# Performance work log

Hardware: AMD Instinct MI355X
Metric: run time of the kernel (lower is better)

## Reference

```python
import jax, jax.numpy as jnp
import numpy as np

B, T, C, E, K = 8, 2048, 1024, 8, 2
CAP = int(T / E * 1.25)  # expert capacity per batch row = 320


def setup_inputs() -> dict:
    key = jax.random.key(0)
    ks = jax.random.split(key, 6)
    s = lambda k, shape, fan: jax.random.normal(k, shape, jnp.float32) / np.sqrt(fan)
    return dict(
        x=jax.random.normal(ks[0], (B, T, C), jnp.float32),
        rw1=s(ks[1], (C, 4 * C), C), rb1=jnp.zeros((4 * C,), jnp.float32),
        rw2=s(ks[2], (4 * C, 4 * C), 4 * C), rb2=jnp.zeros((4 * C,), jnp.float32),
        rw3=s(ks[3], (4 * C, E), 4 * C), rb3=jnp.zeros((E,), jnp.float32),
        ew1=s(ks[4], (E, C, 4 * C), C), eb1=jnp.zeros((E, 4 * C), jnp.float32),
        ew2=s(ks[5], (E, 4 * C, C), 4 * C), eb2=jnp.zeros((E, C), jnp.float32),
    )


def reference(x, rw1, rb1, rw2, rb2, rw3, rb3, ew1, eb1, ew2, eb2):
    # Router (dropout is identity in eval): MLP -> softmax over experts
    h = jax.nn.relu(x @ rw1 + rb1)
    h = jax.nn.relu(h @ rw2 + rb2)
    probs = jax.nn.softmax(h @ rw3 + rb3, axis=-1)        # [B,T,E]
    topk_p, topk_e = jax.lax.top_k(probs, K)              # [B,T,K]

    b_ids = jnp.broadcast_to(jnp.arange(B)[:, None], (B, T))
    out = jnp.zeros_like(x)
    # Loop over small fixed number of experts (mirrors per-rank expert compute)
    for e in range(E):
        sel = (topk_e == e)                               # [B,T,K]
        mask = sel.any(-1)                                # token routed to expert e
        gate = (topk_p * sel).sum(-1)                     # unnormalized top-k prob
        pos = jnp.cumsum(mask, axis=1) - 1                # slot within capacity buffer
        keep = mask & (pos < CAP)                         # capacity truncation (drop overflow)
        pos_s = jnp.where(keep, pos, CAP)                 # CAP is out-of-range -> dropped
        # Dispatch: scatter kept tokens into [B, CAP, C] capacity-padded buffer
        buf = jnp.zeros((B, CAP, C), x.dtype).at[b_ids, pos_s].set(x, mode='drop')
        # Expert FFN on padded buffer
        y = jax.nn.relu(buf @ ew1[e] + eb1[e]) @ ew2[e] + eb2[e]
        # Combine: gather back to token positions, weight by gate
        g = y[b_ids, jnp.where(keep, pos, 0)]
        out = out + gate[..., None] * jnp.where(keep[..., None], g, jnp.zeros((), x.dtype))
    return out
```

## Files before the change

### kernel.cpp

```cpp
#include <hip/hip_runtime.h>
#include <stdint.h>

typedef _Float16 f16;
typedef _Float16 half8 __attribute__((ext_vector_type(8)));
typedef float f32x4 __attribute__((ext_vector_type(4)));

#define NF_MAX 2048
#define THETA  0.02f

__device__ __forceinline__ void gload16(const void* g, void* l) {
  __builtin_amdgcn_global_load_lds(
      (const __attribute__((address_space(1))) void*)g,
      (__attribute__((address_space(3))) void*)l, 16, 0, 0);
}

#define BAR() do { __builtin_amdgcn_s_barrier(); __builtin_amdgcn_sched_barrier(0); } while (0)
#define WAIT_VM8() do { asm volatile("s_waitcnt vmcnt(8)" ::: "memory"); __builtin_amdgcn_sched_barrier(0); } while (0)
#define WAIT_VM0() do { asm volatile("s_waitcnt vmcnt(0)" ::: "memory"); __builtin_amdgcn_sched_barrier(0); } while (0)

template<int EPI, bool SPLIT3>
__launch_bounds__(512, 2)
__global__ void gemm256(const f16* __restrict__ A0, const f16* __restrict__ A1,
                        const f16* __restrict__ B0, const f16* __restrict__ B1,
                        int N, int Kd, int lda, int ldb,
                        const int* __restrict__ rowsrcA, const f16* __restrict__ zeroPage,
                        const float* __restrict__ bias, int bias_stride, int rows_per_exp,
                        f16* __restrict__ oH, int ldo, float* __restrict__ oAcc,
                        const float* __restrict__ w3, float* __restrict__ oLog,
                        const int* __restrict__ nfp)
{
  __shared__ f16 lds[4 * 8192 * 2 + 512];
  f16* sA = lds;
  f16* sB = lds + 4 * 8192;
  f16* sDummy = lds + 8 * 8192;

  const int tid  = threadIdx.x;
  const int lane = tid & 63, w = tid >> 6;
  const int wm = w >> 2, wn = w & 3;

  const int gx  = gridDim.x, gy = gridDim.y;
  const int bid = blockIdx.y * gx + blockIdx.x;
  int by, bx;
  const int scols = gx >> 3;
  const int nst   = scols * (gy >> 2);
  if ((gx & 7) == 0 && (gy & 3) == 0 && (nst & 7) == 0) {
    const int x = bid & 7, j = bid >> 3;
    const int r = j >> 5, jp = j & 31;
    const int s = r * 8 + x;
    const int srow = s / scols, scol = s - srow * scols;
    by = srow * 4 + (jp >> 3);
    bx = scol * 8 + (jp & 7);
  } else {
    const int nwg = gx * gy;
    const int swz = (bid & 7) * (nwg >> 3) + (bid >> 3);
    by = swz / gx; bx = swz - by * gx;
  }
  const int m0  = by * 256, n0 = bx * 256;
  const int k0  = blockIdx.z * Kd;

  if (nfp) {
    int nf = *nfp; nf = nf < NF_MAX ? nf : NF_MAX;
    const int lim = (nf + 255) & ~255;
    if (m0 >= lim) return;
  }

  int e = 0;
  if (rows_per_exp > 0) e = m0 / rows_per_exp;
  const f16* Bh = B0 + (size_t)e * N * ldb;

  const int nk  = Kd >> 6;
  const int NIT = SPLIT3 ? 3 * nk : nk;

  const int sr  = lane & 15;
  const int sk8 = lane >> 4;

  size_t aoff[2], boff[2];
  bool az[2] = { false, false };
  #pragma unroll
  for (int jj = 0; jj < 2; ++jj) {
    const int arow = m0 + (jj * 8 + w) * 16 + sr;
    if (rowsrcA) {
      const int rs = rowsrcA[arow];
      az[jj] = (rs < 0);
      aoff[jj] = az[jj] ? 0 : (size_t)rs * lda;
    } else {
      aoff[jj] = (size_t)arow * lda;
    }
    boff[jj] = (size_t)(n0 + (jj * 8 + w) * 16 + sr) * ldb;
  }

  auto stageA = [&](const f16* base, int kk, int kc, f16* slotBase, bool valid) {
    #pragma unroll
    for (int jj = 0; jj < 2; ++jj) {
      const int mt = jj * 8 + w;
      f16* dst = valid ? (slotBase + mt * 512) : sDummy;
      const f16* src = az[jj] ? zeroPage
                              : base + aoff[jj] + (k0 + kk + kc * 32 + sk8 * 8);
      gload16(src, dst);
    }
  };
  auto stageB = [&](const f16* base, int kk, int kc, f16* slotBase, bool valid) {
    #pragma unroll
    for (int jj = 0; jj < 2; ++jj) {
      const int mt = jj * 8 + w;
      f16* dst = valid ? (slotBase + mt * 512) : sDummy;
      const f16* src = base + boff[jj] + (k0 + kk + kc * 32 + sk8 * 8);
      gload16(src, dst);
    }
  };

  struct It { const f16* Ab; const f16* Bb; int kk, kin, pass; };
  const f16* Ab0 = SPLIT3 ? A1 : A0;
  auto advance = [&](It& s) {
    if (s.kin + 1 < nk) { s.kin++; }
    else if (SPLIT3 && s.pass < 2) {
      s.kin = 0; s.pass++;
      s.Ab = (s.pass == 0) ? A1 : A0;
      s.Bb = (s.pass == 1) ? B1 : Bh;
    }
    s.kk = s.kin << 6;
  };
  It it1 = { Ab0, Bh, 64, 1, 0 };
  It it2 = { Ab0, Bh, 128, 2, 0 };

  stageA(Ab0, 0, 0, &sA[0], true);
  stageB(Bh,  0, 0, &sB[0], true);
  stageA(Ab0, 0, 1, &sA[8192], true);
  stageB(Bh,  0, 1, &sB[8192], true);
  stageA(it1.Ab, it1.kk, 0, &sA[2 * 8192], true);
  stageB(it1.Bb, it1.kk, 0, &sB[2 * 8192], true);
  WAIT_VM8();
  BAR();

  f32x4 acc[8][4] = {};
  const int aBase = wm * 8;
  const int bBase = wn * 4;

  auto mfma16 = [&](half8* af, half8* bf, int moff) {
    __builtin_amdgcn_s_setprio(1);
    #pragma unroll
    for (int mi = 0; mi < 4; ++mi)
      #pragma unroll
      for (int ni = 0; ni < 4; ++ni)
        acc[moff + mi][ni] = __builtin_amdgcn_mfma_f32_16x16x32_f16(
            af[mi], bf[ni], acc[moff + mi][ni], 0, 0, 0);
    __builtin_amdgcn_s_setprio(0);
  };
  auto rdA = [&](half8* dst, int slot, int mtb) {
    #pragma unroll
    for (int mi = 0; mi < 4; ++mi)
      dst[mi] = *(const half8*)&sA[slot * 8192 + (mtb + mi) * 512 + lane * 8];
  };
  auto rdB = [&](half8* dst, int slot) {
    #pragma unroll
    for (int ni = 0; ni < 4; ++ni)
      dst[ni] = *(const half8*)&sB[slot * 8192 + (bBase + ni) * 512 + lane * 8];
  };

  for (int t = 0; t < NIT; ++t) {
    const int sa0 = (2 * t) & 3, sa1 = sa0 ^ 1;
    const bool v1 = (t + 1 < NIT), v2 = (t + 2 < NIT);

    if (SPLIT3 && t == 2 * nk) {
      #pragma unroll
      for (int mi = 0; mi < 8; ++mi)
        #pragma unroll
        for (int ni = 0; ni < 4; ++ni)
          acc[mi][ni] = acc[mi][ni] * 2.44140625e-4f;
    }

    half8 aF[4], bF[4], aG[4];

    rdA(aF, sa0, aBase);
    rdB(bF, sa0);
    stageA(it1.Ab, it1.kk, 1, &sA[(sa0 ^ 3) * 8192], v1);
    BAR();
    mfma16(aF, bF, 0);
    BAR();

    rdA(aG, sa0, aBase + 4);
    stageB(it1.Bb, it1.kk, 1, &sB[(sa0 ^ 3) * 8192], v1);
    WAIT_VM8();
    BAR();
    mfma16(aG, bF, 4);
    BAR();

    rdA(aF, sa1, aBase);
    rdB(bF, sa1);
    stageA(it2.Ab, it2.kk, 0, &sA[sa0 * 8192], v2);
    BAR();
    mfma16(aF, bF, 0);
    BAR();

    rdA(aG, sa1, aBase + 4);
    stageB(it2.Bb, it2.kk, 0, &sB[sa0 * 8192], v2);
    WAIT_VM8();
    BAR();
    mfma16(aG, bF, 4);
    BAR();

    it1 = it2;
    advance(it2);
  }
  WAIT_VM0();

  float bv[4] = { 0.f, 0.f, 0.f, 0.f };
  if (bias) {
    #pragma unroll
    for (int ni = 0; ni < 4; ++ni) {
      const int col = n0 + wn * 64 + ni * 16 + (lane & 15);
      bv[ni] = bias[(size_t)e * bias_stride + col];
    }
  }

  if (EPI == 2) {
    f32x4 wlo[4], whi[4];
    #pragma unroll
    for (int ni = 0; ni < 4; ++ni) {
      const int col = n0 + wn * 64 + ni * 16 + (lane & 15);
      wlo[ni] = *(const f32x4*)(w3 + (size_t)col * 8);
      whi[ni] = *(const f32x4*)(w3 + (size_t)col * 8 + 4);
    }
    const int p = (n0 >> 8) * 4 + wn;
    #pragma unroll
    for (int mi = 0; mi < 8; ++mi) {
      #pragma unroll
      for (int r = 0; r < 4; ++r) {
        const int row = m0 + wm * 128 + mi * 16 + (lane >> 4) * 4 + r;
        f32x4 plo = {}, phi = {};
        #pragma unroll
        for (int ni = 0; ni < 4; ++ni) {
          const float v = fmaxf(acc[mi][ni][r] + bv[ni], 0.f);
          plo += v * wlo[ni];
          phi += v * whi[ni];
        }
        #pragma unroll
        for (int msk = 1; msk < 16; msk <<= 1) {
          #pragma unroll
          for (int q = 0; q < 4; ++q) {
            plo[q] += __shfl_xor(plo[q], msk);
            phi[q] += __shfl_xor(phi[q], msk);
          }
        }
        if ((lane & 15) == 0) {
          float* dst = oLog + ((size_t)p * ldo + row) * 8;
          *(f32x4*)dst = plo;
          *(f32x4*)(dst + 4) = phi;
        }
      }
    }
  } else {
    #pragma unroll
    for (int mi = 0; mi < 8; ++mi) {
      #pragma unroll
      for (int r = 0; r < 4; ++r) {
        const int row = m0 + wm * 128 + mi * 16 + (lane >> 4) * 4 + r;
        #pragma unroll
        for (int ni = 0; ni < 4; ++ni) {
          const int col = n0 + wn * 64 + ni * 16 + (lane & 15);
          if (EPI == 3) {
            atomicAdd(&oAcc[(size_t)row * ldo + col], acc[mi][ni][r]);
          } else {
            float v = acc[mi][ni][r] + bv[ni];
            if (EPI == 0) v = fmaxf(v, 0.f);
            oH[(size_t)row * ldo + col] = (f16)v;
          }
        }
      }
    }
  }
}

__global__ void split_x(const float* __restrict__ x, f16* __restrict__ hi,
                        f16* __restrict__ lo, int n)
{
  const int i = blockIdx.x * 256 + threadIdx.x;
  if (i * 8 >= n) return;
  const f32x4 a = ((const f32x4*)x)[2 * i];
  const f32x4 b = ((const f32x4*)x)[2 * i + 1];
  half8 h, l;
  #pragma unroll
  for (int j = 0; j < 4; ++j) {
    float v = a[j]; f16 hh = (f16)v;
    h[j] = hh; l[j] = (f16)((v - (float)hh) * 4096.0f);
    v = b[j]; hh = (f16)v;
    h[4 + j] = hh; l[4 + j] = (f16)((v - (float)hh) * 4096.0f);
  }
  ((half8*)hi)[i] = h;
  ((half8*)lo)[i] = l;
}

template<bool SPLIT>
__global__ void transpose_conv(const float* __restrict__ in, f16* __restrict__ oh,
                               f16* __restrict__ ol, int R, int Cc)
{
  __shared__ float tile[64][65];
  const size_t boff = (size_t)blockIdx.z * R * Cc;
  in += boff; oh += boff;
  if (SPLIT) ol += boff;
  const int c0 = blockIdx.x * 64, r0 = blockIdx.y * 64;
  #pragma unroll
  for (int i = 0; i < 16; ++i) {
    const int idx = i * 256 + threadIdx.x;
    const int r = idx >> 6, c = idx & 63;
    tile[r][c] = in[(size_t)(r0 + r) * Cc + (c0 + c)];
  }
  __syncthreads();
  #pragma unroll
  for (int i = 0; i < 16; ++i) {
    const int idx = i * 256 + threadIdx.x;
    const int ro = idx >> 6, co = idx & 63;
    const float v = tile[co][ro];
    const f16 h = (f16)v;
    const size_t o = (size_t)(c0 + ro) * R + (r0 + co);
    oh[o] = h;
    if (SPLIT) ol[o] = (f16)((v - (float)h) * 4096.0f);
  }
}

__global__ void topk_flag(const float* __restrict__ part, const float* __restrict__ b3,
                          int* __restrict__ eidx, float* __restrict__ gval,
                          int* __restrict__ flags, int* __restrict__ nfc)
{
  const int t = blockIdx.x * 256 + threadIdx.x;
  float l[8];
  #pragma unroll
  for (int e = 0; e < 8; ++e) l[e] = b3[e];
  for (int p = 0; p < 64; ++p) {
    const float* src = part + ((size_t)p * 16384 + t) * 8;
    const f32x4 a = *(const f32x4*)src;
    const f32x4 b = *(const f32x4*)(src + 4);
    #pragma unroll
    for (int q = 0; q < 4; ++q) { l[q] += a[q]; l[4 + q] += b[q]; }
  }
  float mx = l[0];
  #pragma unroll
  for (int e = 1; e < 8; ++e) mx = fmaxf(mx, l[e]);
  float ex[8], s = 0.f;
  #pragma unroll
  for (int e = 0; e < 8; ++e) { ex[e] = expf(l[e] - mx); s += ex[e]; }
  float p1 = -1.f, p2 = -1.f; int e1 = 0, e2 = 0;
  #pragma unroll
  for (int e = 0; e < 8; ++e) {
    const float pe = ex[e] / s;
    if (pe > p1)      { p2 = p1; e2 = e1; p1 = pe; e1 = e; }
    else if (pe > p2) { p2 = pe; e2 = e; }
  }
  eidx[t * 2] = e1; eidx[t * 2 + 1] = e2;
  gval[t * 2] = p1; gval[t * 2 + 1] = p2;
  float l1 = -1e30f, l2 = -1e30f, l3 = -1e30f;
  #pragma unroll
  for (int e = 0; e < 8; ++e) {
    const float le = l[e];
    if (le > l1)      { l3 = l2; l2 = l1; l1 = le; }
    else if (le > l2) { l3 = l2; l2 = le; }
    else if (le > l3) { l3 = le; }
  }
  if (l2 - l3 < THETA) {
    const int s0 = atomicAdd(nfc, 1);
    if (s0 < NF_MAX) flags[s0] = t;
  }
}

__global__ void post1(const float* __restrict__ h1r, const float* __restrict__ b1,
                      f16* __restrict__ hh, f16* __restrict__ hl,
                      const int* __restrict__ nfc)
{
  int nf = *nfc; nf = nf < NF_MAX ? nf : NF_MAX;
  const int lim = (nf + 255) & ~255;
  const int row = blockIdx.x;
  if (row >= lim) return;
  const int j = blockIdx.y * 2048 + threadIdx.x * 8;
  const float* src = h1r + (size_t)row * 4096 + j;
  const f32x4 a = *(const f32x4*)src;
  const f32x4 b = *(const f32x4*)(src + 4);
  half8 h, l;
  #pragma unroll
  for (int k = 0; k < 4; ++k) {
    float v = fmaxf(a[k] + b1[j + k], 0.f);
    f16 x = (f16)v; h[k] = x; l[k] = (f16)((v - (float)x) * 4096.0f);
    v = fmaxf(b[k] + b1[j + 4 + k], 0.f);
    x = (f16)v; h[4 + k] = x; l[4 + k] = (f16)((v - (float)x) * 4096.0f);
  }
  *(half8*)(hh + (size_t)row * 4096 + j) = h;
  *(half8*)(hl + (size_t)row * 4096 + j) = l;
}

__global__ void logits_exact(const float* __restrict__ h2r, const float* __restrict__ b2,
                             const float* __restrict__ w3, const float* __restrict__ b3,
                             const int* __restrict__ flags, const int* __restrict__ nfc,
                             int* __restrict__ eidx, float* __restrict__ gval)
{
  const int srow = blockIdx.x;
  int nf = *nfc; nf = nf < NF_MAX ? nf : NF_MAX;
  if (srow >= nf) return;
  const float* hrow = h2r + (size_t)srow * 4096;
  double p[8];
  #pragma unroll
  for (int e = 0; e < 8; ++e) p[e] = 0.0;
  for (int i = 0; i < 16; ++i) {
    const int k = i * 256 + threadIdx.x;
    const double h = (double)fmaxf(hrow[k] + b2[k], 0.f);
    const float* wp = w3 + (size_t)k * 8;
    #pragma unroll
    for (int e = 0; e < 8; ++e) p[e] += h * (double)wp[e];
  }
  #pragma unroll
  for (int e = 0; e < 8; ++e)
    for (int off = 32; off > 0; off >>= 1)
      p[e] += __shfl_down(p[e], off);
  __shared__ double sp[4][8];
  const int lane = threadIdx.x & 63, wv = threadIdx.x >> 6;
  if (lane == 0) {
    #pragma unroll
    for (int e = 0; e < 8; ++e) sp[wv][e] = p[e];
  }
  __syncthreads();
  if (threadIdx.x == 0) {
    float l[8];
    #pragma unroll
    for (int e = 0; e < 8; ++e)
      l[e] = (float)(sp[0][e] + sp[1][e] + sp[2][e] + sp[3][e] + (double)b3[e]);
    float mx = l[0];
    for (int e = 1; e < 8; ++e) mx = fmaxf(mx, l[e]);
    float ex[8], s = 0.f;
    for (int e = 0; e < 8; ++e) { ex[e] = expf(l[e] - mx); s += ex[e]; }
    float p1 = -1.f, p2 = -1.f; int e1 = 0, e2 = 0;
    for (int e = 0; e < 8; ++e) {
      const float pe = ex[e] / s;
      if (pe > p1)      { p2 = p1; e2 = e1; p1 = pe; e1 = e; }
      else if (pe > p2) { p2 = pe; e2 = e; }
    }
    const int tok = flags[srow];
    eidx[tok * 2] = e1; eidx[tok * 2 + 1] = e2;
    gval[tok * 2] = p1; gval[tok * 2 + 1] = p2;
  }
}

__global__ void route_scan(const int* __restrict__ eidx, const float* __restrict__ gval,
                           int* __restrict__ cnt, int* __restrict__ rowsrc,
                           int* __restrict__ tokslot)
{
  const int pair = blockIdx.x;
  const int e = pair >> 3, b = pair & 7;
  const int lane = threadIdx.x;
  int running = 0;
  for (int t0 = 0; t0 < 2048; t0 += 64) {
    const int t = t0 + lane;
    const int i2 = (b * 2048 + t) * 2;
    const int m0 = (eidx[i2] == e), m1 = (eidx[i2 + 1] == e);
    const int m = m0 | m1;
    const unsigned long long bal = __ballot(m);
    const int pos = running + __popcll(bal & ((1ull << lane) - 1ull));
    if (m && pos < 320) {
      const int slot = pair * 320 + pos;
      rowsrc[slot] = b * 2048 + t;
      tokslot[(b * 2048 + t) * 2 + (m0 ? 0 : 1)] = slot;
    }
    running += __popcll(bal);
  }
  const int c = running < 320 ? running : 320;
  for (int s = c + lane; s < 320; s += 64) rowsrc[pair * 320 + s] = -1;
  if (lane == 0) cnt[pair] = c;
}

__global__ void combine(const f16* __restrict__ yb, const int* __restrict__ tokslot,
                        const float* __restrict__ gval, float* __restrict__ out)
{
  const int t = blockIdx.x;
  const int s0 = tokslot[t * 2], s1 = tokslot[t * 2 + 1];
  const float g0 = gval[t * 2], g1 = gval[t * 2 + 1];
  float a[8] = {};
  if (s0 >= 0) {
    const half8 y = ((const half8*)(yb + (size_t)s0 * 1024))[threadIdx.x];
    #pragma unroll
    for (int k = 0; k < 8; ++k) a[k] += g0 * (float)y[k];
  }
  if (s1 >= 0) {
    const half8 y = ((const half8*)(yb + (size_t)s1 * 1024))[threadIdx.x];
    #pragma unroll
    for (int k = 0; k < 8; ++k) a[k] += g1 * (float)y[k];
  }
  float* dst = out + (size_t)t * 1024 + threadIdx.x * 8;
  f32x4 lo = { a[0], a[1], a[2], a[3] }, hi = { a[4], a[5], a[6], a[7] };
  *(f32x4*)dst = lo;
  *(f32x4*)(dst + 4) = hi;
}

extern "C" void kernel_launch(void* const* d_in, const int* in_sizes, int n_in,
                              void* d_out, int out_size, void* d_ws, size_t ws_size,
                              hipStream_t stream)
{
  (void)in_sizes; (void)n_in; (void)out_size;
  const float* x   = (const float*)d_in[0];
  const float* rw1 = (const float*)d_in[1];
  const float* rb1 = (const float*)d_in[2];
  const float* rw2 = (const float*)d_in[3];
  const float* rb2 = (const float*)d_in[4];
  const float* rw3 = (const float*)d_in[5];
  const float* rb3 = (const float*)d_in[6];
  const float* ew1 = (const float*)d_in[7];
  const float* eb1 = (const float*)d_in[8];
  const float* ew2 = (const float*)d_in[9];
  const float* eb2 = (const float*)d_in[10];

  constexpr size_t MB = 1024ull * 1024ull;
  constexpr size_t KB = 1024ull;
  char* ws = (char*)d_ws;
  if (ws_size < 401 * MB) return;

  f16*   h1f  = (f16*)(ws);
  f16*   ew1t = (f16*)(ws);
  f16*   ew2t = (f16*)(ws + 64 * MB);
  f16*   xhi  = (f16*)(ws + 128 * MB);
  char*  S    = ws + 160 * MB;
  int*   eidx   = (int*)(S);
  float* gval   = (float*)(S + 128 * KB);
  int*   cnt    = (int*)(S + 256 * KB);
  int*   nfc    = (int*)(S + 260 * KB);
  int*   flags  = (int*)(S + 264 * KB);
  int*   tokslot= (int*)(S + 272 * KB);
  int*   rowsrc = (int*)(S + 400 * KB);
  f16*   zeros  = (f16*)(S + 480 * KB);
  f16*   xlo    = (f16*)(ws + 161 * MB);
  f16*   rw1thi = (f16*)(ws + 193 * MB);
  f16*   rw1tlo = (f16*)(ws + 201 * MB);
  f16*   rw2thi = (f16*)(ws + 209 * MB);
  f16*   rw2tlo = (f16*)(ws + 241 * MB);
  float* part   = (float*)(ws + 273 * MB);
  float* h1r    = (float*)(ws + 305 * MB);
  float* h2r    = (float*)(ws + 337 * MB);
  f16*   h1rh   = (f16*)(ws + 369 * MB);
  f16*   h1rl   = (f16*)(ws + 385 * MB);
  f16*   h_e    = (f16*)(ws + 161 * MB);
  f16*   yb     = (f16*)(ws + 321 * MB);

  hipMemsetAsync(nfc, 0, 4, stream);
  hipMemsetAsync(tokslot, 0xFF, 128 * KB, stream);
  hipMemsetAsync(zeros, 0, 16 * KB, stream);
  hipMemsetAsync(h1r, 0, 64 * MB, stream);

  split_x<<<8192, 256, 0, stream>>>(x, xhi, xlo, 16384 * 1024);
  transpose_conv<true ><<<dim3(64, 16, 1), 256, 0, stream>>>(rw1, rw1thi, rw1tlo, 1024, 4096);
  transpose_conv<true ><<<dim3(64, 64, 1), 256, 0, stream>>>(rw2, rw2thi, rw2tlo, 4096, 4096);

  gemm256<0, false><<<dim3(16, 64), 512, 0, stream>>>(
      xhi, nullptr, rw1thi, nullptr, 4096, 1024, 1024, 1024,
      nullptr, nullptr, rb1, 0, 0,
      h1f, 4096, nullptr, nullptr, nullptr, nullptr);
  gemm256<2, false><<<dim3(16, 64), 512, 0, stream>>>(
      h1f, nullptr, rw2thi, nullptr, 4096, 4096, 4096, 4096,
      nullptr, nullptr, rb2, 0, 0,
      nullptr, 16384, nullptr, rw3, part, nullptr);
  topk_flag<<<64, 256, 0, stream>>>(part, rb3, eidx, gval, flags, nfc);

  gemm256<3, true><<<dim3(16, 8, 2), 512, 0, stream>>>(
      xhi, xlo, rw1thi, rw1tlo, 4096, 512, 1024, 1024,
      flags, zeros, nullptr, 0, 0,
      nullptr, 4096, h1r, nullptr, nullptr, nfc);
  post1<<<dim3(2048, 2), 256, 0, stream>>>(h1r, rb1, h1rh, h1rl, nfc);
  gemm256<3, true><<<dim3(16, 8, 4), 512, 0, stream>>>(
      h1rh, h1rl, rw2thi, rw2tlo, 4096, 1024, 4096, 4096,
      nullptr, nullptr, nullptr, 0, 0,
      nullptr, 4096, h2r, nullptr, nullptr, nfc);
  logits_exact<<<NF_MAX, 256, 0, stream>>>(h2r, rb2, rw3, rb3, flags, nfc,
                                           eidx, gval);

  route_scan<<<64, 64, 0, stream>>>(eidx, gval, cnt, rowsrc, tokslot);

  transpose_conv<false><<<dim3(64, 16, 8), 256, 0, stream>>>(ew1, ew1t, nullptr, 1024, 4096);
  transpose_conv<false><<<dim3(16, 64, 8), 256, 0, stream>>>(ew2, ew2t, nullptr, 4096, 1024);

  gemm256<0, false><<<dim3(16, 80), 512, 0, stream>>>(
      xhi, nullptr, ew1t, nullptr, 4096, 1024, 1024, 1024,
      rowsrc, zeros, eb1, 4096, 2560,
      h_e, 4096, nullptr, nullptr, nullptr, nullptr);
  gemm256<1, false><<<dim3(4, 80), 512, 0, stream>>>(
      h_e, nullptr, ew2t, nullptr, 1024, 4096, 4096, 4096,
      nullptr, nullptr, eb2, 1024, 2560,
      yb, 1024, nullptr, nullptr, nullptr, nullptr);

  combine<<<16384, 128, 0, stream>>>(yb, tokslot, gval, (float*)d_out);
}
```

Measured before the change: 1.766 ms.

## Switch GEMM to 256x128 tiles with 4 waves and 3-stage LDS ring

Replaces the 256x256 tile, 8-wave GEMM with a 256x128 tile computed by 4 waves. Each wave now holds a 128x64 accumulator and issues 32 MFMAs per LDS read phase. The 4-slot double-half pipeline becomes a 3-slot ring with a simpler per-iteration staging schedule. Grid widths double to match the narrower tiles. The aim is to cut LDS use, allow more blocks per CU and reduce barrier overhead, at the cost of lower B-tile reuse per block and less prefetch depth.

```diff
diff --git a/kernel.cpp b/kernel.cpp
--- a/kernel.cpp
+++ b/kernel.cpp
@@ -15,28 +15,27 @@
 }
 
 #define BAR() do { __builtin_amdgcn_s_barrier(); __builtin_amdgcn_sched_barrier(0); } while (0)
-#define WAIT_VM8() do { asm volatile("s_waitcnt vmcnt(8)" ::: "memory"); __builtin_amdgcn_sched_barrier(0); } while (0)
+#define WAIT_VM6() do { asm volatile("s_waitcnt vmcnt(6)" ::: "memory"); __builtin_amdgcn_sched_barrier(0); } while (0)
 #define WAIT_VM0() do { asm volatile("s_waitcnt vmcnt(0)" ::: "memory"); __builtin_amdgcn_sched_barrier(0); } while (0)
 
 template<int EPI, bool SPLIT3>
-__launch_bounds__(512, 2)
-__global__ void gemm256(const f16* __restrict__ A0, const f16* __restrict__ A1,
-                        const f16* __restrict__ B0, const f16* __restrict__ B1,
-                        int N, int Kd, int lda, int ldb,
-                        const int* __restrict__ rowsrcA, const f16* __restrict__ zeroPage,
-                        const float* __restrict__ bias, int bias_stride, int rows_per_exp,
-                        f16* __restrict__ oH, int ldo, float* __restrict__ oAcc,
-                        const float* __restrict__ w3, float* __restrict__ oLog,
-                        const int* __restrict__ nfp)
-{
-  __shared__ f16 lds[4 * 8192 * 2 + 512];
+__launch_bounds__(256, 2)
+__global__ void gemmT(const f16* __restrict__ A0, const f16* __restrict__ A1,
+                      const f16* __restrict__ B0, const f16* __restrict__ B1,
+                      int N, int Kd, int lda, int ldb,
+                      const int* __restrict__ rowsrcA, const f16* __restrict__ zeroPage,
+                      const float* __restrict__ bias, int bias_stride, int rows_per_exp,
+                      f16* __restrict__ oH, int ldo, float* __restrict__ oAcc,
+                      const float* __restrict__ w3, float* __restrict__ oLog,
+                      const int* __restrict__ nfp)
+{
+  __shared__ f16 lds[3 * 8192 + 3 * 4096 + 512];
   f16* sA = lds;
-  f16* sB = lds + 4 * 8192;
-  f16* sDummy = lds + 8 * 8192;
-
-  const int tid  = threadIdx.x;
-  const int lane = tid & 63, w = tid >> 6;
-  const int wm = w >> 2, wn = w & 3;
+  f16* sB = lds + 3 * 8192;
+  f16* sDummy = lds + 3 * 8192 + 3 * 4096;
+
+  const int lane = threadIdx.x & 63, w = threadIdx.x >> 6;
+  const int wm = w >> 1, wn = w & 1;
 
   const int gx  = gridDim.x, gy = gridDim.y;
   const int bid = blockIdx.y * gx + blockIdx.x;
@@ -55,7 +54,7 @@
     const int swz = (bid & 7) * (nwg >> 3) + (bid >> 3);
     by = swz / gx; bx = swz - by * gx;
   }
-  const int m0  = by * 256, n0 = bx * 256;
+  const int m0  = by * 256, n0 = bx * 128;
   const int k0  = blockIdx.z * Kd;
 
   if (nfp) {
@@ -74,25 +73,28 @@
   const int sr  = lane & 15;
   const int sk8 = lane >> 4;
 
-  size_t aoff[2], boff[2];
-  bool az[2] = { false, false };
-  #pragma unroll
-  for (int jj = 0; jj < 2; ++jj) {
-    const int arow = m0 + (jj * 8 + w) * 16 + sr;
+  size_t aoff[4]; bool az[4];
+  #pragma unroll
+  for (int jj = 0; jj < 4; ++jj) {
+    const int arow = m0 + (jj * 4 + w) * 16 + sr;
     if (rowsrcA) {
       const int rs = rowsrcA[arow];
       az[jj] = (rs < 0);
       aoff[jj] = az[jj] ? 0 : (size_t)rs * lda;
     } else {
+      az[jj] = false;
       aoff[jj] = (size_t)arow * lda;
     }
-    boff[jj] = (size_t)(n0 + (jj * 8 + w) * 16 + sr) * ldb;
-  }
+  }
+  size_t boff[2];
+  #pragma unroll
+  for (int jj = 0; jj < 2; ++jj)
+    boff[jj] = (size_t)(n0 + (jj * 4 + w) * 16 + sr) * ldb;
 
   auto stageA = [&](const f16* base, int kk, int kc, f16* slotBase, bool valid) {
     #pragma unroll
-    for (int jj = 0; jj < 2; ++jj) {
-      const int mt = jj * 8 + w;
+    for (int jj = 0; jj < 4; ++jj) {
+      const int mt = jj * 4 + w;
       f16* dst = valid ? (slotBase + mt * 512) : sDummy;
       const f16* src = az[jj] ? zeroPage
                               : base + aoff[jj] + (k0 + kk + kc * 32 + sk8 * 8);
@@ -102,7 +104,7 @@
   auto stageB = [&](const f16* base, int kk, int kc, f16* slotBase, bool valid) {
     #pragma unroll
     for (int jj = 0; jj < 2; ++jj) {
-      const int mt = jj * 8 + w;
+      const int mt = jj * 4 + w;
       f16* dst = valid ? (slotBase + mt * 512) : sDummy;
       const f16* src = base + boff[jj] + (k0 + kk + kc * 32 + sk8 * 8);
       gload16(src, dst);
@@ -121,46 +123,40 @@
     s.kk = s.kin << 6;
   };
   It it1 = { Ab0, Bh, 64, 1, 0 };
-  It it2 = { Ab0, Bh, 128, 2, 0 };
 
   stageA(Ab0, 0, 0, &sA[0], true);
   stageB(Bh,  0, 0, &sB[0], true);
   stageA(Ab0, 0, 1, &sA[8192], true);
-  stageB(Bh,  0, 1, &sB[8192], true);
-  stageA(it1.Ab, it1.kk, 0, &sA[2 * 8192], true);
-  stageB(it1.Bb, it1.kk, 0, &sB[2 * 8192], true);
-  WAIT_VM8();
+  stageB(Bh,  0, 1, &sB[4096], true);
+  WAIT_VM6();
   BAR();
 
   f32x4 acc[8][4] = {};
   const int aBase = wm * 8;
   const int bBase = wn * 4;
 
-  auto mfma16 = [&](half8* af, half8* bf, int moff) {
+  auto mfma32 = [&](half8* a8, half8* bf) {
     __builtin_amdgcn_s_setprio(1);
     #pragma unroll
-    for (int mi = 0; mi < 4; ++mi)
+    for (int mi = 0; mi < 8; ++mi)
       #pragma unroll
       for (int ni = 0; ni < 4; ++ni)
-        acc[moff + mi][ni] = __builtin_amdgcn_mfma_f32_16x16x32_f16(
-            af[mi], bf[ni], acc[moff + mi][ni], 0, 0, 0);
+        acc[mi][ni] = __builtin_amdgcn_mfma_f32_16x16x32_f16(
+            a8[mi], bf[ni], acc[mi][ni], 0, 0, 0);
     __builtin_amdgcn_s_setprio(0);
   };
-  auto rdA = [&](half8* dst, int slot, int mtb) {
-    #pragma unroll
-    for (int mi = 0; mi < 4; ++mi)
-      dst[mi] = *(const half8*)&sA[slot * 8192 + (mtb + mi) * 512 + lane * 8];
+  auto rdA = [&](half8* dst, int slot) {
+    #pragma unroll
+    for (int mi = 0; mi < 8; ++mi)
+      dst[mi] = *(const half8*)&sA[slot * 8192 + (aBase + mi) * 512 + lane * 8];
   };
   auto rdB = [&](half8* dst, int slot) {
     #pragma unroll
     for (int ni = 0; ni < 4; ++ni)
-      dst[ni] = *(const half8*)&sB[slot * 8192 + (bBase + ni) * 512 + lane * 8];
+      dst[ni] = *(const half8*)&sB[slot * 4096 + (bBase + ni) * 512 + lane * 8];
   };
 
   for (int t = 0; t < NIT; ++t) {
-    const int sa0 = (2 * t) & 3, sa1 = sa0 ^ 1;
-    const bool v1 = (t + 1 < NIT), v2 = (t + 2 < NIT);
-
     if (SPLIT3 && t == 2 * nk) {
       #pragma unroll
       for (int mi = 0; mi < 8; ++mi)
@@ -169,38 +165,29 @@
           acc[mi][ni] = acc[mi][ni] * 2.44140625e-4f;
     }
 
-    half8 aF[4], bF[4], aG[4];
-
-    rdA(aF, sa0, aBase);
-    rdB(bF, sa0);
-    stageA(it1.Ab, it1.kk, 1, &sA[(sa0 ^ 3) * 8192], v1);
+    const int s0 = (2 * t) % 3, s1 = (2 * t + 1) % 3, s2 = (2 * t + 2) % 3;
+    const bool v = (t + 1 < NIT);
+    half8 aF[8], bF[4];
+
+    rdA(aF, s0);
+    rdB(bF, s0);
+    stageA(it1.Ab, it1.kk, 0, &sA[s2 * 8192], v);
+    stageB(it1.Bb, it1.kk, 0, &sB[s2 * 4096], v);
+    WAIT_VM6();
     BAR();
-    mfma16(aF, bF, 0);
+    mfma32(aF, bF);
     BAR();
 
-    rdA(aG, sa0, aBase + 4);
-    stageB(it1.Bb, it1.kk, 1, &sB[(sa0 ^ 3) * 8192], v1);
-    WAIT_VM8();
+    rdA(aF, s1);
+    rdB(bF, s1);
+    stageA(it1.Ab, it1.kk, 1, &sA[s0 * 8192], v);
+    stageB(it1.Bb, it1.kk, 1, &sB[s0 * 4096], v);
+    WAIT_VM6();
     BAR();
-    mfma16(aG, bF, 4);
+    mfma32(aF, bF);
     BAR();
 
-    rdA(aF, sa1, aBase);
-    rdB(bF, sa1);
-    stageA(it2.Ab, it2.kk, 0, &sA[sa0 * 8192], v2);
-    BAR();
-    mfma16(aF, bF, 0);
-    BAR();
-
-    rdA(aG, sa1, aBase + 4);
-    stageB(it2.Bb, it2.kk, 0, &sB[sa0 * 8192], v2);
-    WAIT_VM8();
-    BAR();
-    mfma16(aG, bF, 4);
-    BAR();
-
-    it1 = it2;
-    advance(it2);
+    advance(it1);
   }
   WAIT_VM0();
 
@@ -221,7 +208,7 @@
       wlo[ni] = *(const f32x4*)(w3 + (size_t)col * 8);
       whi[ni] = *(const f32x4*)(w3 + (size_t)col * 8 + 4);
     }
-    const int p = (n0 >> 8) * 4 + wn;
+    const int p = (n0 >> 7) * 2 + wn;
     #pragma unroll
     for (int mi = 0; mi < 8; ++mi) {
       #pragma unroll
@@ -544,22 +531,22 @@
   transpose_conv<true ><<<dim3(64, 16, 1), 256, 0, stream>>>(rw1, rw1thi, rw1tlo, 1024, 4096);
   transpose_conv<true ><<<dim3(64, 64, 1), 256, 0, stream>>>(rw2, rw2thi, rw2tlo, 4096, 4096);
 
-  gemm256<0, false><<<dim3(16, 64), 512, 0, stream>>>(
+  gemmT<0, false><<<dim3(32, 64), 256, 0, stream>>>(
       xhi, nullptr, rw1thi, nullptr, 4096, 1024, 1024, 1024,
       nullptr, nullptr, rb1, 0, 0,
       h1f, 4096, nullptr, nullptr, nullptr, nullptr);
-  gemm256<2, false><<<dim3(16, 64), 512, 0, stream>>>(
+  gemmT<2, false><<<dim3(32, 64), 256, 0, stream>>>(
       h1f, nullptr, rw2thi, nullptr, 4096, 4096, 4096, 4096,
       nullptr, nullptr, rb2, 0, 0,
       nullptr, 16384, nullptr, rw3, part, nullptr);
   topk_flag<<<64, 256, 0, stream>>>(part, rb3, eidx, gval, flags, nfc);
 
-  gemm256<3, true><<<dim3(16, 8, 2), 512, 0, stream>>>(
+  gemmT<3, true><<<dim3(32, 8, 2), 256, 0, stream>>>(
       xhi, xlo, rw1thi, rw1tlo, 4096, 512, 1024, 1024,
       flags, zeros, nullptr, 0, 0,
       nullptr, 4096, h1r, nullptr, nullptr, nfc);
   post1<<<dim3(2048, 2), 256, 0, stream>>>(h1r, rb1, h1rh, h1rl, nfc);
-  gemm256<3, true><<<dim3(16, 8, 4), 512, 0, stream>>>(
+  gemmT<3, true><<<dim3(32, 8, 4), 256, 0, stream>>>(
       h1rh, h1rl, rw2thi, rw2tlo, 4096, 1024, 4096, 4096,
       nullptr, nullptr, nullptr, 0, 0,
       nullptr, 4096, h2r, nullptr, nullptr, nfc);
@@ -571,11 +558,11 @@
   transpose_conv<false><<<dim3(64, 16, 8), 256, 0, stream>>>(ew1, ew1t, nullptr, 1024, 4096);
   transpose_conv<false><<<dim3(16, 64, 8), 256, 0, stream>>>(ew2, ew2t, nullptr, 4096, 1024);
 
-  gemm256<0, false><<<dim3(16, 80), 512, 0, stream>>>(
+  gemmT<0, false><<<dim3(32, 80), 256, 0, stream>>>(
       xhi, nullptr, ew1t, nullptr, 4096, 1024, 1024, 1024,
       rowsrc, zeros, eb1, 4096, 2560,
       h_e, 4096, nullptr, nullptr, nullptr, nullptr);
-  gemm256<1, false><<<dim3(4, 80), 512, 0, stream>>>(
+  gemmT<1, false><<<dim3(8, 80), 256, 0, stream>>>(
       h_e, nullptr, ew2t, nullptr, 1024, 4096, 4096, 4096,
       nullptr, nullptr, eb2, 1024, 2560,
       yb, 1024, nullptr, nullptr, nullptr, nullptr);
```

Result: slower. 2.071 ms (+17.3%).
